# Kernel tuning notes

Hardware: AMD Instinct MI355X
Metric: run time of the kernel (lower is better)

## Reference

```python
import jax, jax.numpy as jnp
import numpy as np

B, SQ, SK, D, H = 4, 2048, 2048, 1024, 16
EPS = 1e-6  # flax LayerNorm default


def layer_norm(x, g, b):
    m = x.mean(-1, keepdims=True)
    var = ((x - m) ** 2).mean(-1, keepdims=True)
    return (x - m) * jax.lax.rsqrt(var + EPS) * g + b


def setup_inputs() -> dict:
    key = jax.random.key(0)
    ks = jax.random.split(key, 16)
    s = 1.0 / np.sqrt(D).astype(np.float32)
    inp = {
        'q': jax.random.normal(ks[0], (B, SQ, D), jnp.float32),
        'k': jax.random.normal(ks[1], (B, SK, D), jnp.float32),
        'v': jax.random.normal(ks[2], (B, SK, D), jnp.float32),
        'mask': jax.random.randint(ks[3], (B, SK), 0, 2).astype(bool),
        'Wq': jax.random.normal(ks[4], (D, D), jnp.float32) * s,
        'bq': jnp.zeros((D,), jnp.float32),
        'Wk': jax.random.normal(ks[5], (D, D), jnp.float32) * s,
        'bk': jnp.zeros((D,), jnp.float32),
        'Wv': jax.random.normal(ks[6], (D, D), jnp.float32) * s,
        'bv': jnp.zeros((D,), jnp.float32),
        'Wo': jax.random.normal(ks[7], (D, D), jnp.float32) * s,
        'bo': jnp.zeros((D,), jnp.float32),
        'g1': jnp.ones((D,), jnp.float32),
        'b1': jnp.zeros((D,), jnp.float32),
        'g2': jnp.ones((D,), jnp.float32),
        'b2': jnp.zeros((D,), jnp.float32),
    }
    return inp


def reference(q, k, v, mask, Wq, bq, Wk, bk, Wv, bv, Wo, bo, g1, b1, g2, b2):
    qp = q @ Wq + bq                      # [B, SQ, D]
    kp = k @ Wk + bk                      # [B, SK, D]
    vp = v @ Wv + bv
    qh = qp.reshape(B, SQ, H, D // H)     # head = slice of last dim (matches scatter)
    kh = kp.reshape(B, SK, H, D // H)
    vh = vp.reshape(B, SK, H, D // H)
    # NOTE: original scales by sqrt(dim_out) (full dim), not head dim
    logits = jnp.einsum('bqhd,bkhd->bhqk', qh, kh) / np.sqrt(D).astype(np.float32)
    m = mask[:, None, None, :]            # [B,1,1,SK] broadcast over heads & queries
    A = jax.nn.softmax(jnp.where(m, logits, -jnp.inf), axis=-1)
    A = jnp.where(jnp.isnan(A), 0.0, A)   # fully-masked rows -> 0 (as in original)
    attn = jnp.einsum('bhqk,bkhd->bqhd', A, vh).reshape(B, SQ, D)  # gather heads
    x = layer_norm(qp + attn, g1, b1)
    out = layer_norm(x + jax.nn.relu(x @ Wo + bo), g2, b2)
    return out
```

## Files before the change

kernel.cpp:

```cpp
#include <hip/hip_runtime.h>

#define B_   4
#define SQS  2048
#define SKS  2048
#define DM   1024
#define H_   16
#define MT   8192

typedef __attribute__((ext_vector_type(8))) short bf16x8;
typedef __attribute__((ext_vector_type(4))) float f32x4;

__device__ __forceinline__ float bf2f(unsigned int u) { return __uint_as_float(u << 16); }
__device__ __forceinline__ unsigned short f2bf(float f) {
  unsigned int u = __float_as_uint(f);
  return (unsigned short)((u + 0x7fffu + ((u >> 16) & 1u)) >> 16);
}
__device__ __forceinline__ unsigned int pk_bf16(float a, float b) {
  return __builtin_amdgcn_perm(__float_as_uint(b) + 0x8000u,
                               __float_as_uint(a) + 0x8000u, 0x07060302u);
}
__device__ __forceinline__ unsigned int pk_trunc(float a, float b) {
  return __builtin_amdgcn_perm(__float_as_uint(b), __float_as_uint(a), 0x07060302u);
}
__device__ __forceinline__ float fexp2(float x) {
#if __has_builtin(__builtin_amdgcn_exp2f)
  return __builtin_amdgcn_exp2f(x);
#else
  return __expf(x * 0.69314718056f);
#endif
}
__device__ __forceinline__ void async16(const void* g, void* l) {
  __builtin_amdgcn_global_load_lds((const __attribute__((address_space(1))) unsigned int*)g,
                                   (__attribute__((address_space(3))) unsigned int*)l,
                                   16, 0, 0);
}
__device__ __forceinline__ void cvt8(uint4 u, float* f) {
  f[0] = bf2f(u.x & 0xffffu); f[1] = bf2f(u.x >> 16);
  f[2] = bf2f(u.y & 0xffffu); f[3] = bf2f(u.y >> 16);
  f[4] = bf2f(u.z & 0xffffu); f[5] = bf2f(u.z >> 16);
  f[6] = bf2f(u.w & 0xffffu); f[7] = bf2f(u.w >> 16);
}
__device__ __forceinline__ int colp(int g) {
  return ((g >> 4) & 1) * 32 + ((g >> 2) & 3) * 8 + ((g >> 5) & 1) * 4 + (g & 3);
}

#define KSCALE 0.0450842200f
#define BIAS_UNMASKED 0.0028151213f

__global__ __launch_bounds__(256)
void prep_all(const float* __restrict__ q, const float* __restrict__ k,
              const float* __restrict__ v, const int* __restrict__ mask,
              const float* __restrict__ Wq, const float* __restrict__ Wk,
              const float* __restrict__ Wv, const float* __restrict__ Wo,
              unsigned short* __restrict__ qi, unsigned short* __restrict__ ki,
              unsigned short* __restrict__ vi,
              unsigned short* __restrict__ Wqt, unsigned short* __restrict__ Wkt,
              unsigned short* __restrict__ Wvt, unsigned short* __restrict__ Wot,
              int* __restrict__ idx, int* __restrict__ cinfo)
{
  __shared__ float s[32][33];
  __shared__ int lcnt;
  const int bx = blockIdx.x, tid = threadIdx.x;
  if (bx < 2048) {
#pragma unroll 1
    for (int it = 0; it < 12; it++) {
      const int i6 = it * 2048 + bx;
      const int which = i6 >> 13, i = i6 & 8191;
      const float* src = (which == 0) ? q : (which == 1) ? k : v;
      unsigned short* dst = (which == 0) ? qi : (which == 1) ? ki : vi;
      size_t o = ((size_t)i * 256 + tid) * 4;
      float4 f = *(const float4*)(src + o);
      uint2 u;
      u.x = pk_bf16(f.x, f.y);
      u.y = pk_bf16(f.z, f.w);
      *(uint2*)(dst + o) = u;
    }
  } else if (bx < 2560) {
#pragma unroll 1
    for (int t8 = 0; t8 < 8; t8++) {
      const int idx2 = t8 * 512 + (bx - 2048);
      const int w = idx2 >> 10, t = idx2 & 1023;
      const int n0 = (t & 31) * 32, k0 = (t >> 5) * 32;
      const float* W = (w == 0) ? Wq : (w == 1) ? Wk : (w == 2) ? Wv : Wo;
      unsigned short* Wt = (w == 0) ? Wqt : (w == 1) ? Wkt : (w == 2) ? Wvt : Wot;
#pragma unroll
      for (int p = 0; p < 4; p++) {
        int c = p * 256 + tid;
        int r = c >> 5, cc = c & 31;
        s[r][cc] = W[(size_t)(k0 + r) * DM + n0 + cc];
      }
      __syncthreads();
#pragma unroll
      for (int p = 0; p < 4; p++) {
        int c = p * 256 + tid;
        int r = c >> 5, cc = c & 31;
        Wt[(size_t)(n0 + r) * DM + k0 + cc] = f2bf(s[cc][r]);
      }
      __syncthreads();
    }
  } else {
    const int b = bx - 2560;
    if (tid == 0) lcnt = 0;
    __syncthreads();
#pragma unroll
    for (int e = 0; e < 8; e++) {
      int kk = tid * 8 + e;
      if (mask[b * SKS + kk]) {
        int j = atomicAdd(&lcnt, 1);
        idx[b * SKS + j] = kk;
      }
    }
    __syncthreads();
    if (tid == 0) cinfo[b] = lcnt;
  }
}

__global__ __launch_bounds__(256)
void qkv_gemm(const unsigned short* __restrict__ A0, const unsigned short* __restrict__ A1,
              const unsigned short* __restrict__ A2,
              const unsigned short* __restrict__ W0, const unsigned short* __restrict__ W1,
              const unsigned short* __restrict__ W2,
              const float* __restrict__ s0, const float* __restrict__ s1,
              const float* __restrict__ s2,
              unsigned short* __restrict__ o0, unsigned short* __restrict__ o1,
              unsigned short* __restrict__ vT)
{
  const int L = blockIdx.x + (blockIdx.y << 3) + (blockIdx.z << 9);
  const int g = L & 7, i5 = L >> 3;
  const int nblk = i5 & 7;
  const int yz = (i5 >> 3) + g * 24;
  const int mblk = yz & 63;
  const int z = yz >> 6;

  const unsigned short* A  = (z == 0) ? A0 : (z == 1) ? A1 : A2;
  const unsigned short* Wt = (z == 0) ? W0 : (z == 1) ? W1 : W2;
  const float* bias        = (z == 0) ? s0 : (z == 1) ? s1 : s2;

  __shared__ short SMEM[2 * 128 * 64];
  short* As = SMEM;
  short* Bs = SMEM + 128 * 64;
  const int tid = threadIdx.x;
  const int m0 = mblk * 128, n0 = nblk * 128;
  const int wave = tid >> 6, ln = tid & 15, qd = (tid & 63) >> 4;
  const int wm = (wave >> 1) * 64, wn = (wave & 1) * 64;

  int srow[4], sgj[4];
#pragma unroll
  for (int u = 0; u < 4; u++) {
    int c = u * 256 + tid;
    srow[u] = c >> 3;
    sgj[u] = ((c & 7) ^ (srow[u] & 7)) * 8;
  }

  f32x4 acc[4][4];
  const f32x4 vzero = {0.f, 0.f, 0.f, 0.f};
#pragma unroll
  for (int i = 0; i < 4; i++)
#pragma unroll
    for (int j = 0; j < 4; j++) acc[i][j] = vzero;

  for (int k0 = 0; k0 < DM; k0 += 64) {
    __syncthreads();
#pragma unroll
    for (int u = 0; u < 4; u++) {
      int c = u * 256 + tid;
      async16(A  + (size_t)(m0 + srow[u]) * DM + k0 + sgj[u], (char*)As + c * 16);
      async16(Wt + (size_t)(n0 + srow[u]) * DM + k0 + sgj[u], (char*)Bs + c * 16);
    }
    __syncthreads();

#pragma unroll
    for (int kk = 0; kk < 2; kk++) {
      const int ch = ((kk * 4 + qd) ^ (ln & 7)) * 8;
      bf16x8 af[4], bfr[4];
#pragma unroll
      for (int i = 0; i < 4; i++)
        af[i] = *(const bf16x8*)(As + (wm + i * 16 + ln) * 64 + ch);
#pragma unroll
      for (int j = 0; j < 4; j++)
        bfr[j] = *(const bf16x8*)(Bs + (wn + j * 16 + ln) * 64 + ch);
#pragma unroll
      for (int i = 0; i < 4; i++)
#pragma unroll
        for (int j = 0; j < 4; j++)
          acc[i][j] = __builtin_amdgcn_mfma_f32_16x16x32_bf16(af[i], bfr[j], acc[i][j], 0, 0, 0);
    }
  }

  if (z != 2) {
    unsigned short* C = (z == 0) ? o0 : o1;
    const float sc = (z == 1) ? KSCALE : 1.0f;
#pragma unroll
    for (int j = 0; j < 4; j++) {
      int col = n0 + wn + j * 16 + ln;
      float bj = bias[col];
#pragma unroll
      for (int i = 0; i < 4; i++) {
        int row = m0 + wm + i * 16 + qd * 4;
#pragma unroll
        for (int r = 0; r < 4; r++)
          C[(size_t)(row + r) * DM + col] = f2bf((acc[i][j][r] + bj) * sc);
      }
    }
  } else {
    __syncthreads();
    short* W = SMEM + (wave << 12);
#pragma unroll
    for (int j = 0; j < 4; j++) {
      int col = n0 + wn + j * 16 + ln;
      float bj = bias[col];
      int d = j * 16 + ln;
#pragma unroll
      for (int i = 0; i < 4; i++) {
        int c = (i & 1) * 8 + qd * 2 + ((i >> 1) & 1);
        int pc = c ^ (ln & 7);
        uint2 u;
        u.x = pk_bf16(acc[i][j][0] + bj, acc[i][j][1] + bj);
        u.y = pk_bf16(acc[i][j][2] + bj, acc[i][j][3] + bj);
        *(uint2*)(W + d * 64 + pc * 4) = u;
      }
    }
    const int h  = 2 * nblk + (wave & 1);
    const int bb = (m0 + wm) >> 11;
    const int kg = (m0 + wm) & 2047;
    const int l  = tid & 63;
    unsigned short* vrow_base = vT + ((size_t)(bb * H_ + h) * 64) * SKS + kg;
#pragma unroll
    for (int it = 0; it < 8; it++) {
      int d = it * 8 + (l >> 3);
      int c2 = (l & 7) * 2;
      int pc0 = c2 ^ (d & 7), pc1 = (c2 + 1) ^ (d & 7);
      uint2 a  = *(const uint2*)(W + d * 64 + pc0 * 4);
      uint2 b2 = *(const uint2*)(W + d * 64 + pc1 * 4);
      uint4 o4 = {a.x, a.y, b2.x, b2.y};
      *(uint4*)(vrow_base + (size_t)d * SKS + c2 * 4) = o4;
    }
  }
}

__global__ __launch_bounds__(256)
void compact_kv(const unsigned short* __restrict__ kpb,
                const unsigned short* __restrict__ vTb,
                const int* __restrict__ idx, const int* __restrict__ cinfo,
                unsigned short* __restrict__ kpc,
                unsigned short* __restrict__ vTc)
{
  const int wave = threadIdx.x >> 6, ln = threadIdx.x & 63;
  const int task = blockIdx.x * 4 + wave;
  if (task < 8192) {
    const int b = task >> 11, j = task & 2047;
    const int cnt = cinfo[b];
    const int pad = (cnt + 63) & ~63;
    if (j >= pad) return;
    unsigned short* dst = kpc + ((size_t)b * SKS + j) * DM;
    if (j < cnt) {
      const unsigned short* src = kpb + ((size_t)b * SKS + idx[b * SKS + j]) * DM;
      uint4 a = *(const uint4*)(src + ln * 16);
      uint4 c = *(const uint4*)(src + ln * 16 + 8);
      *(uint4*)(dst + ln * 16)     = a;
      *(uint4*)(dst + ln * 16 + 8) = c;
    } else {
      uint4 zz = {0u, 0u, 0u, 0u};
      *(uint4*)(dst + ln * 16)     = zz;
      *(uint4*)(dst + ln * 16 + 8) = zz;
    }
  } else {
    const int t2 = task - 8192;
    const int b = t2 >> 10;
    const int cnt = cinfo[b];
    const int pad = (cnt + 63) & ~63;
    const unsigned short* src = vTb + (size_t)t2 * SKS;
    unsigned short* dst = vTc + (size_t)t2 * SKS;
    const int cl = colp(ln);
    const int* idxb = idx + b * SKS;
#pragma unroll 1
    for (int j0 = 0; j0 < pad; j0 += 64) {
      int j = j0 + ln;
      unsigned short v = 0;
      if (j < cnt) {
        int kk = idxb[j];
        v = src[(kk & ~63) + colp(kk & 63)];
      }
      dst[j0 + cl] = v;
    }
  }
}

__global__ __launch_bounds__(256)
void gemm_bf16(const unsigned short* __restrict__ A,
               const unsigned short* __restrict__ Wt,
               const float* __restrict__ bias,
               unsigned short* __restrict__ C,
               int relu)
{
  const int L = blockIdx.x + (blockIdx.y << 3);
  const int g = L & 7, i5 = L >> 3;
  const int nblk = i5 & 7;
  const int mblk = (i5 >> 3) + (g << 3);

  __shared__ short As[128 * 64];
  __shared__ short Bs[128 * 64];
  const int tid = threadIdx.x;
  const int m0 = mblk * 128, n0 = nblk * 128;
  const int wave = tid >> 6, ln = tid & 15, qd = (tid & 63) >> 4;
  const int wm = (wave >> 1) * 64, wn = (wave & 1) * 64;

  int srow[4], sgj[4];
#pragma unroll
  for (int u = 0; u < 4; u++) {
    int c = u * 256 + tid;
    srow[u] = c >> 3;
    sgj[u] = ((c & 7) ^ (srow[u] & 7)) * 8;
  }

  f32x4 acc[4][4];
  const f32x4 vzero = {0.f, 0.f, 0.f, 0.f};
#pragma unroll
  for (int i = 0; i < 4; i++)
#pragma unroll
    for (int j = 0; j < 4; j++) acc[i][j] = vzero;

  for (int k0 = 0; k0 < DM; k0 += 64) {
    __syncthreads();
#pragma unroll
    for (int u = 0; u < 4; u++) {
      int c = u * 256 + tid;
      async16(A  + (size_t)(m0 + srow[u]) * DM + k0 + sgj[u], (char*)As + c * 16);
      async16(Wt + (size_t)(n0 + srow[u]) * DM + k0 + sgj[u], (char*)Bs + c * 16);
    }
    __syncthreads();

#pragma unroll
    for (int kk = 0; kk < 2; kk++) {
      const int ch = ((kk * 4 + qd) ^ (ln & 7)) * 8;
      bf16x8 af[4], bfr[4];
#pragma unroll
      for (int i = 0; i < 4; i++)
        af[i] = *(const bf16x8*)(As + (wm + i * 16 + ln) * 64 + ch);
#pragma unroll
      for (int j = 0; j < 4; j++)
        bfr[j] = *(const bf16x8*)(Bs + (wn + j * 16 + ln) * 64 + ch);
#pragma unroll
      for (int i = 0; i < 4; i++)
#pragma unroll
        for (int j = 0; j < 4; j++)
          acc[i][j] = __builtin_amdgcn_mfma_f32_16x16x32_bf16(af[i], bfr[j], acc[i][j], 0, 0, 0);
    }
  }

#pragma unroll
  for (int j = 0; j < 4; j++) {
    int col = n0 + wn + j * 16 + ln;
    float bj = bias[col];
#pragma unroll
    for (int i = 0; i < 4; i++) {
      int row = m0 + wm + i * 16 + qd * 4;
#pragma unroll
      for (int r = 0; r < 4; r++) {
        float v = acc[i][j][r] + bj;
        if (relu) v = fmaxf(v, 0.f);
        C[(size_t)(row + r) * DM + col] = f2bf(v);
      }
    }
  }
}

__global__ __launch_bounds__(256, 4)
void attn_fwd(const unsigned short* __restrict__ qp,
              const unsigned short* __restrict__ kpc,
              const unsigned short* __restrict__ vTc,
              const int* __restrict__ cinfo,
              unsigned short* __restrict__ O0,
              float* __restrict__ lws)
{
  __shared__ __align__(16) short Ks[2][64 * 64];
  __shared__ __align__(16) short Vs[2][64 * 64];

  const int tid = threadIdx.x;
  const int L = blockIdx.x + (blockIdx.y << 4) + (blockIdx.z << 8);
  const int g = L & 7, i5 = L >> 3;
  const int qblk = i5 & 15;
  const int bh = (i5 >> 4) + (g << 3);
  const int h = bh & 15, b = bh >> 4;
  const int q0 = qblk * 128;
  const int wave = tid >> 6, ln = tid & 15, qd = (tid & 63) >> 4;

  const int cnt = cinfo[b];
  const int NT = (cnt + 63) >> 6;

  int sRow[2], sOff[2];
#pragma unroll
  for (int u = 0; u < 2; u++) {
    int c = u * 256 + tid;
    sRow[u] = c >> 3;
    sOff[u] = ((c & 7) ^ (sRow[u] & 7)) * 8;
  }

  const unsigned short* kbase = kpc + (size_t)(b * SKS) * DM + (h << 6);
  const unsigned short* vbase = vTc + (size_t)((b * H_ + h) * 64) * SKS;

  bf16x8 qf[2][2];
#pragma unroll
  for (int gq = 0; gq < 2; gq++) {
    const unsigned short* qrow =
        qp + (size_t)(b * SQS + q0 + wave * 32 + gq * 16 + ln) * DM + (h << 6);
    qf[gq][0] = *(const bf16x8*)(qrow + qd * 8);
    qf[gq][1] = *(const bf16x8*)(qrow + 32 + qd * 8);
  }

  union { bf16x8 v; unsigned int u[4]; } onesf;
  onesf.u[0] = onesf.u[1] = onesf.u[2] = onesf.u[3] = 0x3F803F80u;

  const f32x4 vzero = {0.f, 0.f, 0.f, 0.f};
  f32x4 oA[2][4], lacc[2];
#pragma unroll
  for (int gq = 0; gq < 2; gq++) {
    lacc[gq] = vzero;
#pragma unroll
    for (int t = 0; t < 4; t++) oA[gq][t] = vzero;
  }

#pragma unroll
  for (int u = 0; u < 2; u++) {
    int c = u * 256 + tid;
    async16(kbase + (size_t)sRow[u] * DM + sOff[u], (char*)Ks[0] + c * 16);
    async16(vbase + (size_t)sRow[u] * SKS + sOff[u], (char*)Vs[0] + c * 16);
  }
  __syncthreads();

#pragma unroll 1
  for (int kt = 0; kt < NT; kt++) {
    const int cur = kt & 1;
    if (kt + 1 < NT) {
      const int k1 = (kt + 1) * 64;
#pragma unroll
      for (int u = 0; u < 2; u++) {
        int c = u * 256 + tid;
        async16(kbase + (size_t)(k1 + sRow[u]) * DM + sOff[u], (char*)Ks[cur ^ 1] + c * 16);
        async16(vbase + (size_t)sRow[u] * SKS + k1 + sOff[u], (char*)Vs[cur ^ 1] + c * 16);
      }
    }
    const short* Ksb = Ks[cur];
    const short* Vsb = Vs[cur];

    bf16x8 pf[2][2];
#pragma unroll
    for (int gq = 0; gq < 2; gq++) {
      f32x4 sS[4];
      __builtin_amdgcn_s_setprio(1);
#pragma unroll
      for (int t = 0; t < 4; t++) {
        const short* krow = Ksb + (t * 16 + ln) * 64;
        bf16x8 kf0 = *(const bf16x8*)(krow + ((0 + qd) ^ (ln & 7)) * 8);
        bf16x8 kf1 = *(const bf16x8*)(krow + ((4 + qd) ^ (ln & 7)) * 8);
        int jb = kt * 64 + t * 16 + qd * 4;
        f32x4 btv;
        btv[0] = (jb + 0 < cnt) ? BIAS_UNMASKED : -1e30f;
        btv[1] = (jb + 1 < cnt) ? BIAS_UNMASKED : -1e30f;
        btv[2] = (jb + 2 < cnt) ? BIAS_UNMASKED : -1e30f;
        btv[3] = (jb + 3 < cnt) ? BIAS_UNMASKED : -1e30f;
        f32x4 a = __builtin_amdgcn_mfma_f32_16x16x32_bf16(kf0, qf[gq][0], btv, 0, 0, 0);
        sS[t]   = __builtin_amdgcn_mfma_f32_16x16x32_bf16(kf1, qf[gq][1], a,   0, 0, 0);
      }
      __builtin_amdgcn_s_setprio(0);
      float p[4][4];
#pragma unroll
      for (int t = 0; t < 4; t++) {
        p[t][0] = fexp2(sS[t][0]);
        p[t][1] = fexp2(sS[t][1]);
        p[t][2] = fexp2(sS[t][2]);
        p[t][3] = fexp2(sS[t][3]);
      }
      union { bf16x8 v; unsigned int u[4]; } P0, P1;
      P0.u[0] = pk_trunc(p[0][0], p[0][1]);
      P0.u[1] = pk_trunc(p[0][2], p[0][3]);
      P0.u[2] = pk_trunc(p[2][0], p[2][1]);
      P0.u[3] = pk_trunc(p[2][2], p[2][3]);
      P1.u[0] = pk_trunc(p[1][0], p[1][1]);
      P1.u[1] = pk_trunc(p[1][2], p[1][3]);
      P1.u[2] = pk_trunc(p[3][0], p[3][1]);
      P1.u[3] = pk_trunc(p[3][2], p[3][3]);
      pf[gq][0] = P0.v;
      pf[gq][1] = P1.v;
      lacc[gq] = __builtin_amdgcn_mfma_f32_16x16x32_bf16(pf[gq][0], onesf.v, lacc[gq], 0, 0, 0);
      lacc[gq] = __builtin_amdgcn_mfma_f32_16x16x32_bf16(pf[gq][1], onesf.v, lacc[gq], 0, 0, 0);
    }

    __builtin_amdgcn_s_setprio(1);
#pragma unroll
    for (int t2 = 0; t2 < 4; t2++) {
      const short* vrow = Vsb + (t2 * 16 + ln) * 64;
      bf16x8 vf0 = *(const bf16x8*)(vrow + (((0 + qd) ^ (ln & 7))) * 8);
      bf16x8 vf1 = *(const bf16x8*)(vrow + (((4 + qd) ^ (ln & 7))) * 8);
#pragma unroll
      for (int gq = 0; gq < 2; gq++) {
        oA[gq][t2] = __builtin_amdgcn_mfma_f32_16x16x32_bf16(pf[gq][0], vf0, oA[gq][t2], 0, 0, 0);
        oA[gq][t2] = __builtin_amdgcn_mfma_f32_16x16x32_bf16(pf[gq][1], vf1, oA[gq][t2], 0, 0, 0);
      }
    }
    __builtin_amdgcn_s_setprio(0);

    __syncthreads();
  }

#pragma unroll
  for (int gq = 0; gq < 2; gq++) {
    int qloc = q0 + wave * 32 + gq * 16 + qd * 4;
    if (ln == 0) {
#pragma unroll
      for (int r = 0; r < 4; r++)
        lws[(size_t)(b * H_ + h) * SQS + qloc + r] = lacc[gq][r];
    }
#pragma unroll
    for (int t2 = 0; t2 < 4; t2++)
#pragma unroll
      for (int r = 0; r < 4; r++) {
        size_t idx2 = (size_t)(b * SQS + qloc + r) * DM + (h << 6) + t2 * 16 + ln;
        O0[idx2] = f2bf(oA[gq][t2][r]);
      }
  }
}

__global__ __launch_bounds__(256)
void ln_merge(const unsigned short* __restrict__ Xa, const unsigned short* __restrict__ O0,
              const float* __restrict__ lws,
              const float* __restrict__ gamma, const float* __restrict__ beta,
              unsigned short* __restrict__ outb)
{
  const int wv = threadIdx.x >> 6, l = threadIdx.x & 63;
  const int row = blockIdx.x * 4 + wv;
  const int b = row >> 11, q = row & 2047;
  const int hh = l >> 2;
  const size_t lidx = (size_t)(b * H_ + hh) * SQS + q;
  float lsum = lws[lidx];
  float linv = (lsum > 0.f) ? 1.0f / lsum : 0.f;

  const size_t base = (size_t)row * DM + l * 16;
  float fa[16], f0[16], v[16];
  cvt8(*(const uint4*)(Xa + base),     fa);
  cvt8(*(const uint4*)(Xa + base + 8), fa + 8);
  cvt8(*(const uint4*)(O0 + base),     f0);
  cvt8(*(const uint4*)(O0 + base + 8), f0 + 8);
  float s = 0.f, s2 = 0.f;
#pragma unroll
  for (int e = 0; e < 16; e++) {
    v[e] = fa[e] + f0[e] * linv;
    s  += v[e];
    s2 += v[e] * v[e];
  }
#pragma unroll
  for (int off = 1; off < 64; off <<= 1) {
    s  += __shfl_xor(s, off);
    s2 += __shfl_xor(s2, off);
  }
  float mean = s * (1.0f / 1024.0f);
  float var  = s2 * (1.0f / 1024.0f) - mean * mean;
  float rstd = rsqrtf(var + 1e-6f);
  const int c = l * 16;
  unsigned int o[8];
#pragma unroll
  for (int e = 0; e < 8; e++) {
    float oa = (v[2 * e]     - mean) * rstd * gamma[c + 2 * e]     + beta[c + 2 * e];
    float ob = (v[2 * e + 1] - mean) * rstd * gamma[c + 2 * e + 1] + beta[c + 2 * e + 1];
    o[e] = pk_bf16(oa, ob);
  }
  uint4 o0v = {o[0], o[1], o[2], o[3]};
  uint4 o1v = {o[4], o[5], o[6], o[7]};
  *(uint4*)(outb + base)     = o0v;
  *(uint4*)(outb + base + 8) = o1v;
}

__global__ __launch_bounds__(256)
void ln_fuse(const unsigned short* __restrict__ Xa, const unsigned short* __restrict__ Xb,
             const float* __restrict__ gamma, const float* __restrict__ beta,
             float* __restrict__ outf)
{
  const int wv = threadIdx.x >> 6, l = threadIdx.x & 63;
  const int row = blockIdx.x * 4 + wv;
  const size_t base = (size_t)row * DM + l * 16;
  float fa[16], fb[16], v[16];
  cvt8(*(const uint4*)(Xa + base),     fa);
  cvt8(*(const uint4*)(Xa + base + 8), fa + 8);
  cvt8(*(const uint4*)(Xb + base),     fb);
  cvt8(*(const uint4*)(Xb + base + 8), fb + 8);
  float s = 0.f, s2 = 0.f;
#pragma unroll
  for (int e = 0; e < 16; e++) {
    v[e] = fa[e] + fb[e];
    s  += v[e];
    s2 += v[e] * v[e];
  }
#pragma unroll
  for (int off = 1; off < 64; off <<= 1) {
    s  += __shfl_xor(s, off);
    s2 += __shfl_xor(s2, off);
  }
  float mean = s * (1.0f / 1024.0f);
  float var  = s2 * (1.0f / 1024.0f) - mean * mean;
  float rstd = rsqrtf(var + 1e-6f);
  const int c = l * 16;
#pragma unroll
  for (int e4 = 0; e4 < 4; e4++) {
    float4 ov;
    ov.x = (v[4 * e4 + 0] - mean) * rstd * gamma[c + 4 * e4 + 0] + beta[c + 4 * e4 + 0];
    ov.y = (v[4 * e4 + 1] - mean) * rstd * gamma[c + 4 * e4 + 1] + beta[c + 4 * e4 + 1];
    ov.z = (v[4 * e4 + 2] - mean) * rstd * gamma[c + 4 * e4 + 2] + beta[c + 4 * e4 + 2];
    ov.w = (v[4 * e4 + 3] - mean) * rstd * gamma[c + 4 * e4 + 3] + beta[c + 4 * e4 + 3];
    *(float4*)(outf + base + 4 * e4) = ov;
  }
}

extern "C" void kernel_launch(void* const* d_in, const int* in_sizes, int n_in,
                              void* d_out, int out_size, void* d_ws, size_t ws_size,
                              hipStream_t stream)
{
  (void)in_sizes; (void)n_in; (void)out_size; (void)ws_size;
  const float* q    = (const float*)d_in[0];
  const float* k    = (const float*)d_in[1];
  const float* v    = (const float*)d_in[2];
  const int*   mask = (const int*)  d_in[3];
  const float* Wq   = (const float*)d_in[4];
  const float* bq   = (const float*)d_in[5];
  const float* Wk   = (const float*)d_in[6];
  const float* bk   = (const float*)d_in[7];
  const float* Wv   = (const float*)d_in[8];
  const float* bv   = (const float*)d_in[9];
  const float* Wo   = (const float*)d_in[10];
  const float* bo   = (const float*)d_in[11];
  const float* g1   = (const float*)d_in[12];
  const float* b1   = (const float*)d_in[13];
  const float* g2   = (const float*)d_in[14];
  const float* b2   = (const float*)d_in[15];

  char* ws = (char*)d_ws;
  const size_t SZ16 = (size_t)16 << 20;
  unsigned short* qi   = (unsigned short*)(ws + 0 * SZ16);
  unsigned short* ki   = (unsigned short*)(ws + 1 * SZ16);
  unsigned short* vi   = (unsigned short*)(ws + 2 * SZ16);
  unsigned short* qpb  = (unsigned short*)(ws + 3 * SZ16);
  unsigned short* kpb  = (unsigned short*)(ws + 4 * SZ16);
  unsigned short* kpc  = (unsigned short*)(ws + 5 * SZ16);
  unsigned short* vTb  = (unsigned short*)(ws + 6 * SZ16);
  unsigned short* Wqt  = (unsigned short*)(ws + 7 * SZ16 + ((size_t)0 << 20));
  unsigned short* Wkt  = (unsigned short*)(ws + 7 * SZ16 + ((size_t)2 << 20));
  unsigned short* Wvt  = (unsigned short*)(ws + 7 * SZ16 + ((size_t)4 << 20));
  unsigned short* Wot  = (unsigned short*)(ws + 7 * SZ16 + ((size_t)6 << 20));
  int*            idxb = (int*)           (ws + 7 * SZ16 + ((size_t)8 << 20));
  int*            cinfo= idxb + B_ * SKS;
  float*          lws  = (float*)         (ws + 7 * SZ16 + ((size_t)9 << 20));
  unsigned short* vTc  = vi;
  unsigned short* O0b  = qi;
  unsigned short* xb   = ki;
  unsigned short* hb   = vTb;

  prep_all     <<<2564,             256, 0, stream>>>(q, k, v, mask, Wq, Wk, Wv, Wo,
                                                      qi, ki, vi, Wqt, Wkt, Wvt, Wot,
                                                      idxb, cinfo);

  qkv_gemm     <<<dim3(8, 64, 3),   256, 0, stream>>>(qi, ki, vi, Wqt, Wkt, Wvt,
                                                      bq, bk, bv, qpb, kpb, vTb);

  compact_kv   <<<3072,             256, 0, stream>>>(kpb, vTb, idxb, cinfo, kpc, vTc);

  attn_fwd     <<<dim3(16, 16, 4),  256, 0, stream>>>(qpb, kpc, vTc, cinfo, O0b, lws);

  ln_merge     <<<2048,             256, 0, stream>>>(qpb, O0b, lws, g1, b1, xb);
  gemm_bf16    <<<dim3(8, 64),      256, 0, stream>>>(xb, Wot, bo, hb, 1);
  ln_fuse      <<<2048,             256, 0, stream>>>(xb, hb, g2, b2, (float*)d_out);
}
```

Baseline: 347.3 us.

## Rewrite QKV GEMM with 256x256 tiles, double-buffered LDS and interleaved MFMA

Replaces the 128x128 QKV projection GEMM with a 512-thread kernel computing 256x256 tiles. It double-buffers the LDS stages so global loads for the next K tile overlap MFMA work, and raises wave priority around the MFMA blocks. The V-transpose epilogue is split into two halves to reuse the staging buffer. The aims are more data reuse per loaded byte and less sync stall, at the cost of 128 KB of LDS per block, more accumulator registers, and fewer blocks (384) to fill the CUs.

```diff
diff --git a/kernel.cpp b/kernel.cpp
--- a/kernel.cpp
+++ b/kernel.cpp
@@ -115,76 +115,110 @@
   }
 }
 
-__global__ __launch_bounds__(256)
-void qkv_gemm(const unsigned short* __restrict__ A0, const unsigned short* __restrict__ A1,
-              const unsigned short* __restrict__ A2,
-              const unsigned short* __restrict__ W0, const unsigned short* __restrict__ W1,
-              const unsigned short* __restrict__ W2,
-              const float* __restrict__ s0, const float* __restrict__ s1,
-              const float* __restrict__ s2,
-              unsigned short* __restrict__ o0, unsigned short* __restrict__ o1,
-              unsigned short* __restrict__ vT)
+__global__ __launch_bounds__(512, 2)
+void qkv256(const unsigned short* __restrict__ A0, const unsigned short* __restrict__ A1,
+            const unsigned short* __restrict__ A2,
+            const unsigned short* __restrict__ W0, const unsigned short* __restrict__ W1,
+            const unsigned short* __restrict__ W2,
+            const float* __restrict__ s0, const float* __restrict__ s1,
+            const float* __restrict__ s2,
+            unsigned short* __restrict__ o0, unsigned short* __restrict__ o1,
+            unsigned short* __restrict__ vT)
 {
-  const int L = blockIdx.x + (blockIdx.y << 3) + (blockIdx.z << 9);
+  __shared__ __align__(16) short As[2][256 * 64];
+  __shared__ __align__(16) short Bs[2][256 * 64];
+
+  const int tid = threadIdx.x;
+  const int L = blockIdx.x + (blockIdx.y << 3);
   const int g = L & 7, i5 = L >> 3;
-  const int nblk = i5 & 7;
-  const int yz = (i5 >> 3) + g * 24;
-  const int mblk = yz & 63;
-  const int z = yz >> 6;
+  const int nblk = i5 & 3;
+  const int zm = (i5 >> 2) + g * 12;
+  const int mblk = zm & 31;
+  const int z = zm >> 5;
 
   const unsigned short* A  = (z == 0) ? A0 : (z == 1) ? A1 : A2;
   const unsigned short* Wt = (z == 0) ? W0 : (z == 1) ? W1 : W2;
   const float* bias        = (z == 0) ? s0 : (z == 1) ? s1 : s2;
 
-  __shared__ short SMEM[2 * 128 * 64];
-  short* As = SMEM;
-  short* Bs = SMEM + 128 * 64;
-  const int tid = threadIdx.x;
-  const int m0 = mblk * 128, n0 = nblk * 128;
+  const int m0 = mblk * 256, n0 = nblk * 256;
   const int wave = tid >> 6, ln = tid & 15, qd = (tid & 63) >> 4;
-  const int wm = (wave >> 1) * 64, wn = (wave & 1) * 64;
-
-  int srow[4], sgj[4];
+  const int wm = (wave >> 2) * 128, wn = (wave & 3) * 64;
+
+  int sRow[4], sOff[4];
 #pragma unroll
   for (int u = 0; u < 4; u++) {
-    int c = u * 256 + tid;
-    srow[u] = c >> 3;
-    sgj[u] = ((c & 7) ^ (srow[u] & 7)) * 8;
-  }
-
-  f32x4 acc[4][4];
+    int c = u * 512 + tid;
+    sRow[u] = c >> 3;
+    sOff[u] = ((c & 7) ^ (sRow[u] & 7)) * 8;
+  }
+
+  f32x4 acc[8][4];
   const f32x4 vzero = {0.f, 0.f, 0.f, 0.f};
 #pragma unroll
-  for (int i = 0; i < 4; i++)
+  for (int i = 0; i < 8; i++)
 #pragma unroll
     for (int j = 0; j < 4; j++) acc[i][j] = vzero;
 
-  for (int k0 = 0; k0 < DM; k0 += 64) {
+#pragma unroll
+  for (int u = 0; u < 4; u++) {
+    async16(A  + (size_t)(m0 + sRow[u]) * DM + sOff[u], (char*)As[0] + (u * 512 + tid) * 16);
+    async16(Wt + (size_t)(n0 + sRow[u]) * DM + sOff[u], (char*)Bs[0] + (u * 512 + tid) * 16);
+  }
+  __syncthreads();
+
+#pragma unroll 1
+  for (int kt = 0; kt < 16; kt++) {
+    const int cur = kt & 1;
+    const short* Asb = As[cur];
+    const short* Bsb = Bs[cur];
+    char* Ad = (char*)As[cur ^ 1];
+    char* Bd = (char*)Bs[cur ^ 1];
+    const bool st = (kt + 1) < 16;
+    const int k1 = (kt + 1) * 64;
+
+    bf16x8 af[4][2], bf[2][2];
+
+#define STG(u)                                                                              \
+    if (st) {                                                                               \
+      async16(A  + (size_t)(m0 + sRow[u]) * DM + k1 + sOff[u], Ad + ((u) * 512 + tid) * 16);\
+      async16(Wt + (size_t)(n0 + sRow[u]) * DM + k1 + sOff[u], Bd + ((u) * 512 + tid) * 16);\
+    }
+#define LD_AF(ih)                                                                           \
+    _Pragma("unroll")                                                                       \
+    for (int i2 = 0; i2 < 4; i2++)                                                          \
+      _Pragma("unroll")                                                                     \
+      for (int kk = 0; kk < 2; kk++)                                                        \
+        af[i2][kk] = *(const bf16x8*)(Asb + (wm + (ih) * 64 + i2 * 16 + ln) * 64 +          \
+                                      ((kk * 4 + qd) ^ (ln & 7)) * 8);
+#define LD_BF(jh)                                                                           \
+    _Pragma("unroll")                                                                       \
+    for (int j2 = 0; j2 < 2; j2++)                                                          \
+      _Pragma("unroll")                                                                     \
+      for (int kk = 0; kk < 2; kk++)                                                        \
+        bf[j2][kk] = *(const bf16x8*)(Bsb + (wn + (jh) * 32 + j2 * 16 + ln) * 64 +          \
+                                      ((kk * 4 + qd) ^ (ln & 7)) * 8);
+#define MM(ih, jh)                                                                          \
+    __builtin_amdgcn_s_setprio(1);                                                         \
+    _Pragma("unroll")                                                                       \
+    for (int i2 = 0; i2 < 4; i2++)                                                          \
+      _Pragma("unroll")                                                                     \
+      for (int j2 = 0; j2 < 2; j2++)                                                        \
+        _Pragma("unroll")                                                                   \
+        for (int kk = 0; kk < 2; kk++)                                                      \
+          acc[(ih) * 4 + i2][(jh) * 2 + j2] = __builtin_amdgcn_mfma_f32_16x16x32_bf16(      \
+              af[i2][kk], bf[j2][kk], acc[(ih) * 4 + i2][(jh) * 2 + j2], 0, 0, 0);          \
+    __builtin_amdgcn_s_setprio(0);
+
+    STG(0); LD_AF(0); LD_BF(0); MM(0, 0);
+    STG(1); LD_AF(1);           MM(1, 0);
+    STG(2);           LD_BF(1); MM(1, 1);
+    STG(3); LD_AF(0);           MM(0, 1);
+
     __syncthreads();
-#pragma unroll
-    for (int u = 0; u < 4; u++) {
-      int c = u * 256 + tid;
-      async16(A  + (size_t)(m0 + srow[u]) * DM + k0 + sgj[u], (char*)As + c * 16);
-      async16(Wt + (size_t)(n0 + srow[u]) * DM + k0 + sgj[u], (char*)Bs + c * 16);
-    }
-    __syncthreads();
-
-#pragma unroll
-    for (int kk = 0; kk < 2; kk++) {
-      const int ch = ((kk * 4 + qd) ^ (ln & 7)) * 8;
-      bf16x8 af[4], bfr[4];
-#pragma unroll
-      for (int i = 0; i < 4; i++)
-        af[i] = *(const bf16x8*)(As + (wm + i * 16 + ln) * 64 + ch);
-#pragma unroll
-      for (int j = 0; j < 4; j++)
-        bfr[j] = *(const bf16x8*)(Bs + (wn + j * 16 + ln) * 64 + ch);
-#pragma unroll
-      for (int i = 0; i < 4; i++)
-#pragma unroll
-        for (int j = 0; j < 4; j++)
-          acc[i][j] = __builtin_amdgcn_mfma_f32_16x16x32_bf16(af[i], bfr[j], acc[i][j], 0, 0, 0);
-    }
+#undef STG
+#undef LD_AF
+#undef LD_BF
+#undef MM
   }
 
   if (z != 2) {
@@ -195,7 +229,7 @@
       int col = n0 + wn + j * 16 + ln;
       float bj = bias[col];
 #pragma unroll
-      for (int i = 0; i < 4; i++) {
+      for (int i = 0; i < 8; i++) {
         int row = m0 + wm + i * 16 + qd * 4;
 #pragma unroll
         for (int r = 0; r < 4; r++)
@@ -204,36 +238,43 @@
     }
   } else {
     __syncthreads();
-    short* W = SMEM + (wave << 12);
-#pragma unroll
-    for (int j = 0; j < 4; j++) {
-      int col = n0 + wn + j * 16 + ln;
-      float bj = bias[col];
-      int d = j * 16 + ln;
-#pragma unroll
-      for (int i = 0; i < 4; i++) {
-        int c = (i & 1) * 8 + qd * 2 + ((i >> 1) & 1);
-        int pc = c ^ (ln & 7);
-        uint2 u;
-        u.x = pk_bf16(acc[i][j][0] + bj, acc[i][j][1] + bj);
-        u.y = pk_bf16(acc[i][j][2] + bj, acc[i][j][3] + bj);
-        *(uint2*)(W + d * 64 + pc * 4) = u;
-      }
-    }
-    const int h  = 2 * nblk + (wave & 1);
-    const int bb = (m0 + wm) >> 11;
-    const int kg = (m0 + wm) & 2047;
+    short* W = (short*)As[0] + (wave << 12);
+    const int h  = nblk * 4 + (wave & 3);
+    const int tb = m0 + wm;
+    const int bb = tb >> 11;
+    const int kgb = tb & 2047;
     const int l  = tid & 63;
-    unsigned short* vrow_base = vT + ((size_t)(bb * H_ + h) * 64) * SKS + kg;
-#pragma unroll
-    for (int it = 0; it < 8; it++) {
-      int d = it * 8 + (l >> 3);
-      int c2 = (l & 7) * 2;
-      int pc0 = c2 ^ (d & 7), pc1 = (c2 + 1) ^ (d & 7);
-      uint2 a  = *(const uint2*)(W + d * 64 + pc0 * 4);
-      uint2 b2 = *(const uint2*)(W + d * 64 + pc1 * 4);
-      uint4 o4 = {a.x, a.y, b2.x, b2.y};
-      *(uint4*)(vrow_base + (size_t)d * SKS + c2 * 4) = o4;
+#pragma unroll 1
+    for (int half = 0; half < 2; half++) {
+#pragma unroll
+      for (int j = 0; j < 4; j++) {
+        int col = n0 + wn + j * 16 + ln;
+        float bj = bias[col];
+        int d = j * 16 + ln;
+#pragma unroll
+        for (int i = 0; i < 4; i++) {
+          int ia = half * 4 + i;
+          int c = (i & 1) * 8 + qd * 2 + ((i >> 1) & 1);
+          int pc = c ^ (ln & 7);
+          uint2 u;
+          u.x = pk_bf16(acc[ia][j][0] + bj, acc[ia][j][1] + bj);
+          u.y = pk_bf16(acc[ia][j][2] + bj, acc[ia][j][3] + bj);
+          *(uint2*)(W + d * 64 + pc * 4) = u;
+        }
+      }
+      __syncthreads();
+      unsigned short* vrow_base = vT + ((size_t)(bb * H_ + h) * 64) * SKS + kgb + half * 64;
+#pragma unroll
+      for (int it = 0; it < 8; it++) {
+        int d = it * 8 + (l >> 3);
+        int c2 = (l & 7) * 2;
+        int pc0 = c2 ^ (d & 7), pc1 = (c2 + 1) ^ (d & 7);
+        uint2 a  = *(const uint2*)(W + d * 64 + pc0 * 4);
+        uint2 b2 = *(const uint2*)(W + d * 64 + pc1 * 4);
+        uint4 o4 = {a.x, a.y, b2.x, b2.y};
+        *(uint4*)(vrow_base + (size_t)d * SKS + c2 * 4) = o4;
+      }
+      __syncthreads();
     }
   }
 }
@@ -657,7 +698,7 @@
                                                       qi, ki, vi, Wqt, Wkt, Wvt, Wot,
                                                       idxb, cinfo);
 
-  qkv_gemm     <<<dim3(8, 64, 3),   256, 0, stream>>>(qi, ki, vi, Wqt, Wkt, Wvt,
+  qkv256       <<<dim3(8, 48),      512, 0, stream>>>(qi, ki, vi, Wqt, Wkt, Wvt,
                                                       bq, bk, bv, qpb, kpb, vTb);
 
   compact_kv   <<<3072,             256, 0, stream>>>(kpb, vTb, idxb, cinfo, kpc, vTc);
```

New measurement: 654.0 us. +88.3%, slower.
